# Performance work log

Measured on AMD Instinct MI355X. Metric: run time of the kernel, lower is better.

Reference implementation:

```python
import jax, jax.numpy as jnp
import numpy as np

B, L, D, K = 64, 4096, 128, 64
ALPHA = 100.0
BN_EPS = 1e-5
L2_EPS = 1e-12


def setup_inputs() -> dict:
    key = jax.random.key(0)
    ks = jax.random.split(key, 6)
    centroids = jax.random.uniform(ks[0], (K, D), dtype=jnp.float32)
    # assignment mapper initialized from centroids (as in _init_params), then
    # treated as independent parameters
    assign_w = 2.0 * ALPHA * centroids
    assign_b = -ALPHA * jnp.linalg.norm(centroids, axis=1)
    x = jax.random.normal(ks[1], (B, L, D), dtype=jnp.float32)
    bn_gamma = jax.random.uniform(ks[2], (K * D,), dtype=jnp.float32)
    bn_beta = jnp.zeros((K * D,), dtype=jnp.float32)
    bn_mean = 0.01 * jax.random.normal(ks[3], (K * D,), dtype=jnp.float32)
    bn_var = jnp.abs(1.0 + 0.1 * jax.random.normal(ks[4], (K * D,), dtype=jnp.float32))
    return {"x": x, "assign_w": assign_w, "assign_b": assign_b,
            "centroids": centroids, "bn_gamma": bn_gamma, "bn_beta": bn_beta,
            "bn_mean": bn_mean, "bn_var": bn_var}


def reference(x, assign_w, assign_b, centroids, bn_gamma, bn_beta, bn_mean, bn_var):
    # descriptor-wise L2 normalization of input
    x = x / jnp.maximum(jnp.linalg.norm(x, axis=2, keepdims=True), L2_EPS)
    # soft assignment: (B, L, K)
    logits = jnp.einsum('bld,kd->blk', x, assign_w) + assign_b
    soft_assign = jax.nn.softmax(logits, axis=2)
    # VLAD pooling, GEMM reformulation of sum_l a[b,l,k]*(x[b,l,:]-c[k,:]):
    # (B, K, D)
    vlad = jnp.einsum('blk,bld->bkd', soft_assign, x) \
        - soft_assign.sum(axis=1)[:, :, None] * centroids[None, :, :]
    # intra-cluster L2 normalization
    vlad = vlad / jnp.maximum(jnp.linalg.norm(vlad, axis=2, keepdims=True), L2_EPS)
    vlad = vlad.reshape(x.shape[0], -1)  # (B, K*D)
    # final BatchNorm1d in inference mode (running stats); dropout inactive in eval
    vlad = bn_gamma * (vlad - bn_mean) * jax.lax.rsqrt(bn_var + BN_EPS) + bn_beta
    return vlad
```

## Files before the change

kernel.cpp:

```cpp
#include <hip/hip_runtime.h>
#include <math.h>

#define NB 64
#define NL 4096
#define ND 128
#define NK 64
#define NS 8
#define LC (NL / NS)
#define LT 64
#define NT (LC / LT)

typedef _Float16 h8 __attribute__((ext_vector_type(8)));
typedef _Float16 h4 __attribute__((ext_vector_type(4)));
typedef float f4 __attribute__((ext_vector_type(4)));

#define MFMA16(A, B, C) __builtin_amdgcn_mfma_f32_16x16x32_f16(A, B, C, 0, 0, 0)
#define QSCALE 2048.0f
#define QINV   4.8828125e-4f

__device__ __forceinline__ int w_idx(int k, int d) {
    return k * 128 + ((((d >> 3) ^ (k & 15)) & 15) << 3) + (d & 7);
}
__device__ __forceinline__ int xt_idx(int d, int c) {
    return d * 64 + ((((c >> 3) ^ (d & 7) ^ ((d >> 3) & 7)) & 7) << 3) + (c & 7);
}
__device__ __forceinline__ int at_idx(int k, int c) {
    return k * 64 + ((((c >> 3) ^ (k & 7)) & 7) << 3) + (c & 7);
}

__global__ __launch_bounds__(256, 2)
void vlad_partial_kernel(const float* __restrict__ x,
                         const float* __restrict__ Wg,
                         const float* __restrict__ bg,
                         float* __restrict__ wsv,
                         float* __restrict__ wsa)
{
    __shared__ __attribute__((aligned(16))) _Float16 sm[40960];
    _Float16* Wh  = sm;
    _Float16* Wl  = sm + 8192;
    _Float16* xTh = sm + 16384;
    _Float16* xTl = sm + 24576;
    _Float16* aTh = sm + 32768;
    _Float16* aTl = sm + 36864;

    const int tid = threadIdx.x;
    const int b = blockIdx.x / NS;
    const int s = blockIdx.x % NS;
    const int l   = tid & 63;
    const int w   = tid >> 6;
    const int l15 = l & 15;
    const int wl4 = l >> 4;

    const float* xb = x + ((size_t)b * NL + (size_t)s * LC) * ND;

    {
        const int k  = tid & 63;
        const int d0 = (tid >> 6) * 32;
        const float4* wr = (const float4*)(Wg + k * ND + d0);
#pragma unroll
        for (int i = 0; i < 8; ++i) {
            float4 wv = wr[i];
            float vv[4] = {wv.x, wv.y, wv.z, wv.w};
            h4 whi, wlo;
#pragma unroll
            for (int j = 0; j < 4; ++j) {
                const _Float16 h = (_Float16)vv[j];
                whi[j] = h;
                wlo[j] = (_Float16)((vv[j] - (float)h) * QSCALE);
            }
            const int id = w_idx(k, d0 + 4 * i);
            *(h4*)(Wh + id) = whi;
            *(h4*)(Wl + id) = wlo;
        }
    }

    float bias[4];
#pragma unroll
    for (int kt = 0; kt < 4; ++kt) bias[kt] = bg[16 * kt + l15];

    const f4 fzero = {0.f, 0.f, 0.f, 0.f};
    f4 P[4][2], Q[4][2];
#pragma unroll
    for (int i = 0; i < 4; ++i)
#pragma unroll
        for (int j = 0; j < 2; ++j) { P[i][j] = fzero; Q[i][j] = fzero; }

    float asum4[4] = {0.f, 0.f, 0.f, 0.f};

    float4 va[4], vb4[4];
    {
        const float* gp = xb + (size_t)(16 * w + l15) * ND + 8 * wl4;
#pragma unroll
        for (int kk = 0; kk < 4; ++kk) {
            va[kk]  = *(const float4*)(gp + 32 * kk);
            vb4[kk] = *(const float4*)(gp + 32 * kk + 4);
        }
    }

    for (int t = 0; t < NT; ++t) {
        float ss = 0.f;
#pragma unroll
        for (int kk = 0; kk < 4; ++kk) {
            ss += va[kk].x * va[kk].x + va[kk].y * va[kk].y +
                  va[kk].z * va[kk].z + va[kk].w * va[kk].w;
            ss += vb4[kk].x * vb4[kk].x + vb4[kk].y * vb4[kk].y +
                  vb4[kk].z * vb4[kk].z + vb4[kk].w * vb4[kk].w;
        }
        ss += __shfl_xor(ss, 16);
        ss += __shfl_xor(ss, 32);
        const float sc = 1.f / fmaxf(sqrtf(ss), 1e-12f);

        h8 xh[4], xl[4];
#pragma unroll
        for (int kk = 0; kk < 4; ++kk) {
            float f[8] = {va[kk].x * sc, va[kk].y * sc, va[kk].z * sc, va[kk].w * sc,
                          vb4[kk].x * sc, vb4[kk].y * sc, vb4[kk].z * sc, vb4[kk].w * sc};
#pragma unroll
            for (int e = 0; e < 8; ++e) {
                const _Float16 h = (_Float16)f[e];
                xh[kk][e] = h;
                xl[kk][e] = (_Float16)((f[e] - (float)h) * QSCALE);
            }
        }

        __syncthreads();

        {
            const int c = 16 * w + l15;
#pragma unroll
            for (int kk = 0; kk < 4; ++kk)
#pragma unroll
                for (int e = 0; e < 8; ++e) {
                    const int d  = 32 * kk + 8 * wl4 + e;
                    const int id = xt_idx(d, c);
                    xTh[id] = xh[kk][e];
                    xTl[id] = xl[kk][e];
                }
        }

        if (t + 1 < NT) {
            const float* gp = xb + (size_t)((t + 1) * LT + 16 * w + l15) * ND + 8 * wl4;
#pragma unroll
            for (int kk = 0; kk < 4; ++kk) {
                va[kk]  = *(const float4*)(gp + 32 * kk);
                vb4[kk] = *(const float4*)(gp + 32 * kk + 4);
            }
        }

        f4 aP[4], aQ[4];
#pragma unroll
        for (int kt = 0; kt < 4; ++kt) { aP[kt] = fzero; aQ[kt] = fzero; }
#pragma unroll
        for (int kk = 0; kk < 4; ++kk) {
#pragma unroll
            for (int kt = 0; kt < 4; ++kt) {
                const int k    = 16 * kt + l15;
                const int base = k * 128 + ((((4 * kk + wl4) ^ (k & 15)) & 15) << 3);
                const h8 wh = *(const h8*)(Wh + base);
                const h8 wl = *(const h8*)(Wl + base);
                aP[kt] = MFMA16(xh[kk], wh, aP[kt]);
                aQ[kt] = MFMA16(xh[kk], wl, aQ[kt]);
                aQ[kt] = MFMA16(xl[kk], wh, aQ[kt]);
            }
        }

        const int crow = 16 * w + 4 * wl4;
        h4 abh[4], abl[4];
#pragma unroll
        for (int r = 0; r < 4; ++r) {
            float v0 = aP[0][r] + aQ[0][r] * QINV + bias[0];
            float v1 = aP[1][r] + aQ[1][r] * QINV + bias[1];
            float v2 = aP[2][r] + aQ[2][r] * QINV + bias[2];
            float v3 = aP[3][r] + aQ[3][r] * QINV + bias[3];
            float m = fmaxf(fmaxf(v0, v1), fmaxf(v2, v3));
            m = fmaxf(m, __shfl_xor(m, 1));
            m = fmaxf(m, __shfl_xor(m, 2));
            m = fmaxf(m, __shfl_xor(m, 4));
            m = fmaxf(m, __shfl_xor(m, 8));
            const float e0 = __expf(v0 - m);
            const float e1 = __expf(v1 - m);
            const float e2 = __expf(v2 - m);
            const float e3 = __expf(v3 - m);
            float smx = e0 + e1 + e2 + e3;
            smx += __shfl_xor(smx, 1);
            smx += __shfl_xor(smx, 2);
            smx += __shfl_xor(smx, 4);
            smx += __shfl_xor(smx, 8);
            const float inv = 1.f / smx;
            const float a0 = e0 * inv, a1 = e1 * inv, a2 = e2 * inv, a3 = e3 * inv;
            asum4[0] += a0; asum4[1] += a1; asum4[2] += a2; asum4[3] += a3;
            const _Float16 h0 = (_Float16)a0, h1 = (_Float16)a1;
            const _Float16 h2 = (_Float16)a2, h3 = (_Float16)a3;
            abh[0][r] = h0; abl[0][r] = (_Float16)((a0 - (float)h0) * QSCALE);
            abh[1][r] = h1; abl[1][r] = (_Float16)((a1 - (float)h1) * QSCALE);
            abh[2][r] = h2; abl[2][r] = (_Float16)((a2 - (float)h2) * QSCALE);
            abh[3][r] = h3; abl[3][r] = (_Float16)((a3 - (float)h3) * QSCALE);
        }
#pragma unroll
        for (int kt = 0; kt < 4; ++kt) {
            const int k  = 16 * kt + l15;
            const int id = k * 64 + ((((crow >> 3) ^ (k & 7)) & 7) << 3) + (crow & 7);
            *(h4*)(aTh + id) = abh[kt];
            *(h4*)(aTl + id) = abl[kt];
        }

        __syncthreads();

#pragma unroll
        for (int st = 0; st < 2; ++st) {
            const int c0 = 32 * st + 8 * wl4;
            h8 ah[4], al[4];
#pragma unroll
            for (int kt = 0; kt < 4; ++kt) {
                const int k    = 16 * kt + l15;
                const int base = k * 64 + ((((c0 >> 3) ^ (k & 7)) & 7) << 3);
                ah[kt] = *(const h8*)(aTh + base);
                al[kt] = *(const h8*)(aTl + base);
            }
#pragma unroll
            for (int dt = 0; dt < 2; ++dt) {
                const int d    = 32 * w + 16 * dt + l15;
                const int base = d * 64 + ((((c0 >> 3) ^ (d & 7) ^ ((d >> 3) & 7)) & 7) << 3);
                const h8 bh = *(const h8*)(xTh + base);
                const h8 bl = *(const h8*)(xTl + base);
#pragma unroll
                for (int kt = 0; kt < 4; ++kt) {
                    P[kt][dt] = MFMA16(ah[kt], bh, P[kt][dt]);
                    Q[kt][dt] = MFMA16(ah[kt], bl, Q[kt][dt]);
                    Q[kt][dt] = MFMA16(al[kt], bh, Q[kt][dt]);
                }
            }
        }
    }

    float* ob = wsv + (size_t)(b * NS + s) * NK * ND;
#pragma unroll
    for (int kt = 0; kt < 4; ++kt)
#pragma unroll
        for (int dt = 0; dt < 2; ++dt)
#pragma unroll
            for (int r = 0; r < 4; ++r) {
                const int k = 16 * kt + 4 * wl4 + r;
                const int d = 32 * w + 16 * dt + l15;
                ob[k * ND + d] = P[kt][dt][r] + Q[kt][dt][r] * QINV;
            }

#pragma unroll
    for (int kt = 0; kt < 4; ++kt) {
        float vv = asum4[kt];
        vv += __shfl_xor(vv, 16);
        vv += __shfl_xor(vv, 32);
        asum4[kt] = vv;
    }
    __syncthreads();
    float* scr = (float*)sm;
    if (l < 16) {
#pragma unroll
        for (int kt = 0; kt < 4; ++kt) scr[w * 64 + 16 * kt + l] = asum4[kt];
    }
    __syncthreads();
    if (tid < NK) {
        wsa[(size_t)(b * NS + s) * NK + tid] =
            scr[tid] + scr[64 + tid] + scr[128 + tid] + scr[192 + tid];
    }
}

__global__ __launch_bounds__(64)
void vlad_finalize_kernel(const float* __restrict__ wsv,
                          const float* __restrict__ wsa,
                          const float* __restrict__ cen,
                          const float* __restrict__ gam,
                          const float* __restrict__ bet,
                          const float* __restrict__ mu,
                          const float* __restrict__ var,
                          float* __restrict__ out)
{
    const int bk = blockIdx.x;
    const int b = bk >> 6;
    const int k = bk & 63;
    const int lane = threadIdx.x;

    const float* vb = wsv + (size_t)b * NS * NK * ND + (size_t)k * ND;
    float v0 = 0.f, v1 = 0.f, as = 0.f;
#pragma unroll
    for (int s = 0; s < NS; ++s) {
        const float* p = vb + (size_t)s * NK * ND;
        v0 += p[lane];
        v1 += p[lane + 64];
        as += wsa[(b * NS + s) * NK + k];
    }
    const int i0 = k * ND + lane;
    const int i1 = i0 + 64;
    v0 -= as * cen[i0];
    v1 -= as * cen[i1];

    float ss = v0 * v0 + v1 * v1;
#pragma unroll
    for (int o = 1; o < 64; o <<= 1) ss += __shfl_xor(ss, o);
    const float sc = 1.f / fmaxf(sqrtf(ss), 1e-12f);

    const float n0 = v0 * sc;
    const float n1 = v1 * sc;
    float* ob = out + (size_t)b * NK * ND;
    ob[i0] = gam[i0] * (n0 - mu[i0]) * rsqrtf(var[i0] + 1e-5f) + bet[i0];
    ob[i1] = gam[i1] * (n1 - mu[i1]) * rsqrtf(var[i1] + 1e-5f) + bet[i1];
}

extern "C" void kernel_launch(void* const* d_in, const int* in_sizes, int n_in,
                              void* d_out, int out_size, void* d_ws, size_t ws_size,
                              hipStream_t stream) {
    const float* x  = (const float*)d_in[0];
    const float* aw = (const float*)d_in[1];
    const float* ab = (const float*)d_in[2];
    const float* ce = (const float*)d_in[3];
    const float* g  = (const float*)d_in[4];
    const float* be = (const float*)d_in[5];
    const float* mu = (const float*)d_in[6];
    const float* va = (const float*)d_in[7];
    float* out = (float*)d_out;

    float* wsv = (float*)d_ws;
    float* wsa = wsv + (size_t)NB * NS * NK * ND;

    hipLaunchKernelGGL(vlad_partial_kernel, dim3(NB * NS), dim3(256), 0, stream,
                       x, aw, ab, wsv, wsa);
    hipLaunchKernelGGL(vlad_finalize_kernel, dim3(NB * NK), dim3(64), 0, stream,
                       wsv, wsa, ce, g, be, mu, va, out);
}
```

Measured before the change: 217.5 us.

## Transpose logits MFMA, drop x low-part in pooling GEMM, cut shared memory

The assignment GEMM now puts W as the A operand, so each lane holds 16 cluster logits for a single row. The softmax reduction becomes mostly in-register, needing only two cross-lane shuffles per max and per sum. The pooling GEMM drops the x low-precision correction term, which removes one third of its MFMAs and the xTl shared buffer. That shrinks LDS use and may allow higher occupancy, but it lowers the precision of the x operand in the VLAD accumulation and adds scalar LDS stores for the assignment tile.

```diff
diff --git a/kernel.cpp b/kernel.cpp
--- a/kernel.cpp
+++ b/kernel.cpp
@@ -24,9 +24,6 @@
 __device__ __forceinline__ int xt_idx(int d, int c) {
     return d * 64 + ((((c >> 3) ^ (d & 7) ^ ((d >> 3) & 7)) & 7) << 3) + (c & 7);
 }
-__device__ __forceinline__ int at_idx(int k, int c) {
-    return k * 64 + ((((c >> 3) ^ (k & 7)) & 7) << 3) + (c & 7);
-}
 
 __global__ __launch_bounds__(256, 2)
 void vlad_partial_kernel(const float* __restrict__ x,
@@ -35,13 +32,12 @@
                          float* __restrict__ wsv,
                          float* __restrict__ wsa)
 {
-    __shared__ __attribute__((aligned(16))) _Float16 sm[40960];
+    __shared__ __attribute__((aligned(16))) _Float16 sm[32768];
     _Float16* Wh  = sm;
     _Float16* Wl  = sm + 8192;
     _Float16* xTh = sm + 16384;
-    _Float16* xTl = sm + 24576;
-    _Float16* aTh = sm + 32768;
-    _Float16* aTl = sm + 36864;
+    _Float16* aTh = sm + 24576;
+    _Float16* aTl = sm + 28672;
 
     const int tid = threadIdx.x;
     const int b = blockIdx.x / NS;
@@ -74,9 +70,10 @@
         }
     }
 
-    float bias[4];
-#pragma unroll
-    for (int kt = 0; kt < 4; ++kt) bias[kt] = bg[16 * kt + l15];
+    float4 bias4[4];
+#pragma unroll
+    for (int kt = 0; kt < 4; ++kt)
+        bias4[kt] = *(const float4*)(bg + 16 * kt + 4 * wl4);
 
     const f4 fzero = {0.f, 0.f, 0.f, 0.f};
     f4 P[4][2], Q[4][2];
@@ -85,7 +82,9 @@
 #pragma unroll
         for (int j = 0; j < 2; ++j) { P[i][j] = fzero; Q[i][j] = fzero; }
 
-    float asum4[4] = {0.f, 0.f, 0.f, 0.f};
+    float asum16[16];
+#pragma unroll
+    for (int i = 0; i < 16; ++i) asum16[i] = 0.f;
 
     float4 va[4], vb4[4];
     {
@@ -96,6 +95,8 @@
             vb4[kk] = *(const float4*)(gp + 32 * kk + 4);
         }
     }
+
+    const int cRow = 16 * w + l15;
 
     for (int t = 0; t < NT; ++t) {
         float ss = 0.f;
@@ -125,18 +126,13 @@
 
         __syncthreads();
 
-        {
-            const int c = 16 * w + l15;
-#pragma unroll
-            for (int kk = 0; kk < 4; ++kk)
-#pragma unroll
-                for (int e = 0; e < 8; ++e) {
-                    const int d  = 32 * kk + 8 * wl4 + e;
-                    const int id = xt_idx(d, c);
-                    xTh[id] = xh[kk][e];
-                    xTl[id] = xl[kk][e];
-                }
-        }
+#pragma unroll
+        for (int kk = 0; kk < 4; ++kk)
+#pragma unroll
+            for (int e = 0; e < 8; ++e) {
+                const int d = 32 * kk + 8 * wl4 + e;
+                xTh[xt_idx(d, cRow)] = xh[kk][e];
+            }
 
         if (t + 1 < NT) {
             const float* gp = xb + (size_t)((t + 1) * LT + 16 * w + l15) * ND + 8 * wl4;
@@ -158,51 +154,46 @@
                 const int base = k * 128 + ((((4 * kk + wl4) ^ (k & 15)) & 15) << 3);
                 const h8 wh = *(const h8*)(Wh + base);
                 const h8 wl = *(const h8*)(Wl + base);
-                aP[kt] = MFMA16(xh[kk], wh, aP[kt]);
-                aQ[kt] = MFMA16(xh[kk], wl, aQ[kt]);
-                aQ[kt] = MFMA16(xl[kk], wh, aQ[kt]);
-            }
-        }
-
-        const int crow = 16 * w + 4 * wl4;
-        h4 abh[4], abl[4];
-#pragma unroll
-        for (int r = 0; r < 4; ++r) {
-            float v0 = aP[0][r] + aQ[0][r] * QINV + bias[0];
-            float v1 = aP[1][r] + aQ[1][r] * QINV + bias[1];
-            float v2 = aP[2][r] + aQ[2][r] * QINV + bias[2];
-            float v3 = aP[3][r] + aQ[3][r] * QINV + bias[3];
-            float m = fmaxf(fmaxf(v0, v1), fmaxf(v2, v3));
-            m = fmaxf(m, __shfl_xor(m, 1));
-            m = fmaxf(m, __shfl_xor(m, 2));
-            m = fmaxf(m, __shfl_xor(m, 4));
-            m = fmaxf(m, __shfl_xor(m, 8));
-            const float e0 = __expf(v0 - m);
-            const float e1 = __expf(v1 - m);
-            const float e2 = __expf(v2 - m);
-            const float e3 = __expf(v3 - m);
-            float smx = e0 + e1 + e2 + e3;
-            smx += __shfl_xor(smx, 1);
-            smx += __shfl_xor(smx, 2);
-            smx += __shfl_xor(smx, 4);
-            smx += __shfl_xor(smx, 8);
-            const float inv = 1.f / smx;
-            const float a0 = e0 * inv, a1 = e1 * inv, a2 = e2 * inv, a3 = e3 * inv;
-            asum4[0] += a0; asum4[1] += a1; asum4[2] += a2; asum4[3] += a3;
-            const _Float16 h0 = (_Float16)a0, h1 = (_Float16)a1;
-            const _Float16 h2 = (_Float16)a2, h3 = (_Float16)a3;
-            abh[0][r] = h0; abl[0][r] = (_Float16)((a0 - (float)h0) * QSCALE);
-            abh[1][r] = h1; abl[1][r] = (_Float16)((a1 - (float)h1) * QSCALE);
-            abh[2][r] = h2; abl[2][r] = (_Float16)((a2 - (float)h2) * QSCALE);
-            abh[3][r] = h3; abl[3][r] = (_Float16)((a3 - (float)h3) * QSCALE);
-        }
-#pragma unroll
-        for (int kt = 0; kt < 4; ++kt) {
-            const int k  = 16 * kt + l15;
-            const int id = k * 64 + ((((crow >> 3) ^ (k & 7)) & 7) << 3) + (crow & 7);
-            *(h4*)(aTh + id) = abh[kt];
-            *(h4*)(aTl + id) = abl[kt];
-        }
+                aP[kt] = MFMA16(wh, xh[kk], aP[kt]);
+                aQ[kt] = MFMA16(wl, xh[kk], aQ[kt]);
+                aQ[kt] = MFMA16(wh, xl[kk], aQ[kt]);
+            }
+        }
+
+        float Lg[16];
+#pragma unroll
+        for (int kt = 0; kt < 4; ++kt)
+#pragma unroll
+            for (int r = 0; r < 4; ++r)
+                Lg[4 * kt + r] = aP[kt][r] + aQ[kt][r] * QINV +
+                                 ((const float*)&bias4[kt])[r];
+
+        float mx = fmaxf(Lg[0], Lg[1]);
+#pragma unroll
+        for (int i = 2; i < 16; ++i) mx = fmaxf(mx, Lg[i]);
+        mx = fmaxf(mx, __shfl_xor(mx, 16));
+        mx = fmaxf(mx, __shfl_xor(mx, 32));
+
+        float ee[16];
+        float sum = 0.f;
+#pragma unroll
+        for (int i = 0; i < 16; ++i) { ee[i] = __expf(Lg[i] - mx); sum += ee[i]; }
+        sum += __shfl_xor(sum, 16);
+        sum += __shfl_xor(sum, 32);
+        const float inv = 1.f / sum;
+
+#pragma unroll
+        for (int kt = 0; kt < 4; ++kt)
+#pragma unroll
+            for (int r = 0; r < 4; ++r) {
+                const float a = ee[4 * kt + r] * inv;
+                asum16[4 * kt + r] += a;
+                const int k  = 16 * kt + 4 * wl4 + r;
+                const int id = k * 64 + ((((cRow >> 3) ^ (k & 7)) & 7) << 3) + (cRow & 7);
+                const _Float16 h = (_Float16)a;
+                aTh[id] = h;
+                aTl[id] = (_Float16)((a - (float)h) * QSCALE);
+            }
 
         __syncthreads();
 
@@ -222,11 +213,9 @@
                 const int d    = 32 * w + 16 * dt + l15;
                 const int base = d * 64 + ((((c0 >> 3) ^ (d & 7) ^ ((d >> 3) & 7)) & 7) << 3);
                 const h8 bh = *(const h8*)(xTh + base);
-                const h8 bl = *(const h8*)(xTl + base);
 #pragma unroll
                 for (int kt = 0; kt < 4; ++kt) {
                     P[kt][dt] = MFMA16(ah[kt], bh, P[kt][dt]);
-                    Q[kt][dt] = MFMA16(ah[kt], bl, Q[kt][dt]);
                     Q[kt][dt] = MFMA16(al[kt], bh, Q[kt][dt]);
                 }
             }
@@ -246,17 +235,22 @@
             }
 
 #pragma unroll
-    for (int kt = 0; kt < 4; ++kt) {
-        float vv = asum4[kt];
-        vv += __shfl_xor(vv, 16);
-        vv += __shfl_xor(vv, 32);
-        asum4[kt] = vv;
+    for (int i = 0; i < 16; ++i) {
+        float vv = asum16[i];
+        vv += __shfl_xor(vv, 1);
+        vv += __shfl_xor(vv, 2);
+        vv += __shfl_xor(vv, 4);
+        vv += __shfl_xor(vv, 8);
+        asum16[i] = vv;
     }
     __syncthreads();
     float* scr = (float*)sm;
-    if (l < 16) {
-#pragma unroll
-        for (int kt = 0; kt < 4; ++kt) scr[w * 64 + 16 * kt + l] = asum4[kt];
+    if (l15 == 0) {
+#pragma unroll
+        for (int kt = 0; kt < 4; ++kt)
+#pragma unroll
+            for (int r = 0; r < 4; ++r)
+                scr[w * 64 + 16 * kt + 4 * wl4 + r] = asum16[4 * kt + r];
     }
     __syncthreads();
     if (tid < NK) {
```

Measured after the change: 218.6 us. About the same (+0.5%).
